# Performance work log

Hardware: AMD Instinct MI355X
Metric: run time of the kernel (lower is better)

The kernel has to match this reference:

```python
import jax, jax.numpy as jnp
import numpy as np

B, L, S, H, E = 2, 2048, 2048, 8, 64
EPS = 1e-8


def setup_inputs() -> dict:
    key = jax.random.key(0)
    k1, k2, k3, k4, k5 = jax.random.split(key, 5)
    query = jax.random.normal(k1, (B, L, H, E), jnp.float32)
    key_t = jax.random.normal(k2, (B, S, H, E), jnp.float32)
    value = jax.random.normal(k3, (B, S, H, E), jnp.float32)
    mask_miss_k = jax.random.bernoulli(k4, 0.1, (B, S, 1))
    mask_miss_q = jax.random.bernoulli(k5, 0.1, (B, L, 1))
    # ensure key position 0 is never missing so no softmax row is fully masked
    mask_miss_k = mask_miss_k.at[:, 0, :].set(False)
    pos = jnp.broadcast_to(jnp.arange(L, dtype=jnp.int32)[None, :, None], (B, L, 1))
    return {"query": query, "key": key_t, "value": value,
            "mask_miss_k": mask_miss_k, "mask_miss_q": mask_miss_q,
            "pos": pos, "causal_mask": 1}


def reference(query, key, value, mask_miss_k, mask_miss_q, pos, causal_mask):
    # query: (B,L,H,E)  key/value: (B,S,H,E)  masks: (B,S,1)/(B,L,1) bool  pos: (B,L,1)
    E_ = query.shape[-1]
    scale = 1.0 / np.sqrt(E_)
    neg_inf = jnp.float32(-jnp.inf)

    scores = jnp.einsum('blhe,bshe->bhls', query, key)  # (B,H,L,S)

    if causal_mask:
        p = pos[..., 0]  # (B,L)
        # M[b,i,j] = -inf where p_j > p_i, broadcast over heads
        m_causal = jnp.where(p[:, None, :] > p[:, :, None], neg_inf, 0.0)[:, None, :, :]
        scores = scores + m_causal

    m_k = jnp.where(mask_miss_k[..., 0][:, None, None, :], neg_inf, 0.0)  # (B,1,1,S)
    m_q = jnp.where(mask_miss_q[..., 0][:, None, :, None], neg_inf, 0.0)  # (B,1,L,1)

    att = jax.nn.relu(jax.nn.softmax(scale * (scores + m_k), axis=-1) + m_q)

    # per-row attention entropy (register_entropy=True path)
    entropy = -jnp.sum(att * jnp.log(jnp.clip(att, EPS, None)), axis=-1)  # (B,H,L)
    entropy = jnp.nan_to_num(entropy, nan=0.0)

    # dropout p=0.0 -> identity; nan_to_num as in original
    A = jnp.nan_to_num(att)
    V = jnp.einsum('bhls,bshd->blhd', A, value)  # (B,L,H,E)
    return V, A, entropy
```

## Files before the change

### kernel.cpp

```cpp
#include <hip/hip_runtime.h>

#define B_ 2
#define L_ 2048
#define S_ 2048
#define H_ 8
#define E_ 64
#define VSTRIDE 136

typedef float f32x4 __attribute__((ext_vector_type(4)));
typedef short s16x8 __attribute__((ext_vector_type(8)));
typedef unsigned int u32;
typedef unsigned short u16;
typedef unsigned long long u64;

__device__ __forceinline__ u32 bc(float f){ return __builtin_bit_cast(u32, f); }
__device__ __forceinline__ float exp2g(float x){ return __builtin_amdgcn_exp2f(x); }

__device__ __forceinline__ s16x8 pack8(f32x4 a, f32x4 b){
  union { s16x8 v; u32 w[4]; } r;
  r.w[0] = __builtin_amdgcn_perm(bc(a[1]), bc(a[0]), 0x07060302u);
  r.w[1] = __builtin_amdgcn_perm(bc(a[3]), bc(a[2]), 0x07060302u);
  r.w[2] = __builtin_amdgcn_perm(bc(b[1]), bc(b[0]), 0x07060302u);
  r.w[3] = __builtin_amdgcn_perm(bc(b[3]), bc(b[2]), 0x07060302u);
  return r.v;
}

__device__ __forceinline__ void loadK2(const float* kr, s16x8& f0, s16x8& f1){
  f32x4 a0 = *(const f32x4*)(kr);
  f32x4 a1 = *(const f32x4*)(kr + 4);
  f32x4 b0 = *(const f32x4*)(kr + 32);
  f32x4 b1 = *(const f32x4*)(kr + 36);
  f0 = pack8(a0, a1);
  f1 = pack8(b0, b1);
}

__launch_bounds__(256, 4)
__global__ void attn_kernel(const float* __restrict__ Q,
                            const float* __restrict__ K,
                            const float* __restrict__ V,
                            const int* __restrict__ maskK,
                            const int* __restrict__ maskQ,
                            const int* __restrict__ causal_p,
                            float* __restrict__ outV,
                            float* __restrict__ outA,
                            float* __restrict__ outEnt)
{
  __shared__ __align__(16) u16 vstage[64 * VSTRIDE];
  __shared__ float lsum[4][32];
  __shared__ float tsum[4][32];
  __shared__ float recipS[32];
  __shared__ __align__(8) unsigned char mkb[2048];

  const int tid  = threadIdx.x;
  const int lane = tid & 63;
  const int wv   = tid >> 6;
  const int quad = lane >> 4;
  const int l15  = lane & 15;
  const int permrow = ((l15 >> 2) << 3) | (l15 & 3);

  const int n   = blockIdx.x;
  const int s   = n >> 3;
  const int bh  = ((n & 7) << 1) | (s >> 6);
  const int b   = bh >> 3;
  const int h   = bh & 7;
  const int iA  = (s & 63) << 4;
  const int iB  = 2032 - iA;

  const int causal = causal_p[0] != 0;
  const int imaxA  = causal ? (iA + 15) : (S_ - 1);
  const int imaxB  = causal ? (iB + 15) : (S_ - 1);
  const int nsup   = (imaxB >> 7) + 1;

  {
    const int* mk = maskK + b * S_ + tid * 8;
    u32 w0 = (u32)(mk[0]!=0) | ((u32)(mk[1]!=0)<<8) | ((u32)(mk[2]!=0)<<16) | ((u32)(mk[3]!=0)<<24);
    u32 w1 = (u32)(mk[4]!=0) | ((u32)(mk[5]!=0)<<8) | ((u32)(mk[6]!=0)<<16) | ((u32)(mk[7]!=0)<<24);
    ((uint2*)mkb)[tid] = make_uint2(w0, w1);
  }

  float* const outArowA = outA + ((size_t)bh * L_ + iA) * S_;
  float* const outArowB = outA + ((size_t)bh * L_ + iB) * S_;

  if (causal){
    const f32x4 z4 = {0.f, 0.f, 0.f, 0.f};
    const int jzA = ((imaxA >> 5) + 1) << 5;
    for (int r = 0; r < 16; ++r)
      for (int c = jzA + (tid << 2); c < S_; c += 1024)
        *(f32x4*)(outArowA + (size_t)r * S_ + c) = z4;
    const int jzB = ((imaxB >> 5) + 1) << 5;
    for (int r = 0; r < 16; ++r)
      for (int c = jzB + (tid << 2); c < S_; c += 1024)
        *(f32x4*)(outArowB + (size_t)r * S_ + c) = z4;
  }

  s16x8 qfA0, qfA1, qfB0, qfB1;
  {
    const float qs = 0.125f * 1.44269504f;
    const float* qa = Q + (((size_t)(b * L_ + iA + l15)) * H_ + h) * E_;
    const float* qb = Q + (((size_t)(b * L_ + iB + l15)) * H_ + h) * E_;
    qfA0 = pack8(*(const f32x4*)(qa + quad*8) * qs,      *(const f32x4*)(qa + quad*8 + 4) * qs);
    qfA1 = pack8(*(const f32x4*)(qa + 32 + quad*8) * qs, *(const f32x4*)(qa + 32 + quad*8 + 4) * qs);
    qfB0 = pack8(*(const f32x4*)(qb + quad*8) * qs,      *(const f32x4*)(qb + quad*8 + 4) * qs);
    qfB1 = pack8(*(const f32x4*)(qb + 32 + quad*8) * qs, *(const f32x4*)(qb + 32 + quad*8 + 4) * qs);
  }

  const float* const Kbh = K + ((size_t)(b * S_) * H_ + h) * E_;
  const f32x4 zero4 = {0.f, 0.f, 0.f, 0.f};
  const int irowA = iA + l15;
  const int irowB = iB + l15;

  __syncthreads();

  float lA = 0.f, tA = 0.f, lB = 0.f, tB = 0.f;
  for (int c = wv; (c << 5) <= imaxB; c += 4){
    const int j0c = c << 5;
    s16x8 ka0, ka1, kb0, kb1;
    const float* krow = Kbh + (size_t)(j0c + permrow) * (H_ * E_) + quad * 8;
    loadK2(krow, ka0, ka1);
    loadK2(krow + 4 * (H_ * E_), kb0, kb1);
    const int jbase = j0c + (quad << 3);
    const u64 mk8 = *(const u64*)(mkb + jbase);
    const u32 mlo = (u32)mk8;
    const u32 mhi = (u32)(mk8 >> 32);
    {
      f32x4 sa = __builtin_amdgcn_mfma_f32_16x16x32_bf16(ka0, qfB0, zero4, 0, 0, 0);
      sa       = __builtin_amdgcn_mfma_f32_16x16x32_bf16(ka1, qfB1, sa, 0, 0, 0);
      f32x4 sb = __builtin_amdgcn_mfma_f32_16x16x32_bf16(kb0, qfB0, zero4, 0, 0, 0);
      sb       = __builtin_amdgcn_mfma_f32_16x16x32_bf16(kb1, qfB1, sb, 0, 0, 0);
      const int rel = irowB - jbase;
      #pragma unroll
      for (int r = 0; r < 4; ++r){
        const bool da = (((mlo >> (8*r)) & 0xffu) != 0u) || (causal && (r > rel));
        const float ea = da ? 0.f : exp2g(sa[r]);
        lB += ea; tB = __builtin_fmaf(ea, sa[r], tB);
        const bool db = (((mhi >> (8*r)) & 0xffu) != 0u) || (causal && (r + 4 > rel));
        const float eb = db ? 0.f : exp2g(sb[r]);
        lB += eb; tB = __builtin_fmaf(eb, sb[r], tB);
      }
    }
    if (j0c <= imaxA){
      f32x4 sa = __builtin_amdgcn_mfma_f32_16x16x32_bf16(ka0, qfA0, zero4, 0, 0, 0);
      sa       = __builtin_amdgcn_mfma_f32_16x16x32_bf16(ka1, qfA1, sa, 0, 0, 0);
      f32x4 sb = __builtin_amdgcn_mfma_f32_16x16x32_bf16(kb0, qfA0, zero4, 0, 0, 0);
      sb       = __builtin_amdgcn_mfma_f32_16x16x32_bf16(kb1, qfA1, sb, 0, 0, 0);
      const int rel = irowA - jbase;
      #pragma unroll
      for (int r = 0; r < 4; ++r){
        const bool da = (((mlo >> (8*r)) & 0xffu) != 0u) || (causal && (r > rel));
        const float ea = da ? 0.f : exp2g(sa[r]);
        lA += ea; tA = __builtin_fmaf(ea, sa[r], tA);
        const bool db = (((mhi >> (8*r)) & 0xffu) != 0u) || (causal && (r + 4 > rel));
        const float eb = db ? 0.f : exp2g(sb[r]);
        lA += eb; tA = __builtin_fmaf(eb, sb[r], tA);
      }
    }
  }

  #pragma unroll
  for (int off = 16; off < 64; off <<= 1){
    lA += __shfl_xor(lA, off);  tA += __shfl_xor(tA, off);
    lB += __shfl_xor(lB, off);  tB += __shfl_xor(tB, off);
  }
  if (lane < 16){
    lsum[wv][l15]      = lA;  tsum[wv][l15]      = tA;
    lsum[wv][16 + l15] = lB;  tsum[wv][16 + l15] = tB;
  }
  __syncthreads();
  if (tid < 32){
    float l = lsum[0][tid] + lsum[1][tid] + lsum[2][tid] + lsum[3][tid];
    float t = (tsum[0][tid] + tsum[1][tid] + tsum[2][tid] + tsum[3][tid]) * 0.69314718f;
    const int i0t = (tid < 16) ? iA : iB;
    const int row = i0t + (tid & 15);
    int qm = maskQ[b * L_ + row];
    float rc  = (qm != 0) ? 0.f : (1.f / l);
    float ent = (qm != 0) ? 0.f : (__logf(l) - t / l);
    recipS[tid] = rc;
    outEnt[(size_t)bh * L_ + row] = ent;
  }
  __syncthreads();

  const float rqA = recipS[l15];
  const float rqB = recipS[16 + l15];

  f32x4 uaccA[4], uaccB[4];
  #pragma unroll
  for (int et = 0; et < 4; ++et){ uaccA[et] = (f32x4)0.f; uaccB[et] = (f32x4)0.f; }

  for (int sp = 0; sp < nsup; ++sp){
    const int j0c = (sp << 7) + (wv << 5);
    if (j0c > imaxB) break;

    {
      const int jp = tid >> 2;
      const int a  = tid & 3;
      const int e0 = a << 4;
      const float* v0 = V + (((size_t)(b * S_ + (sp << 7) + 2 * jp)) * H_ + h) * E_ + e0;
      const float* v1 = v0 + H_ * E_;
      f32x4 x0 = *(const f32x4*)(v0);
      f32x4 x1 = *(const f32x4*)(v0 + 4);
      f32x4 x2 = *(const f32x4*)(v0 + 8);
      f32x4 x3 = *(const f32x4*)(v0 + 12);
      f32x4 y0 = *(const f32x4*)(v1);
      f32x4 y1 = *(const f32x4*)(v1 + 4);
      f32x4 y2 = *(const f32x4*)(v1 + 8);
      f32x4 y3 = *(const f32x4*)(v1 + 12);
      const int colsw = ((((jp >> 2) + (a << 2)) & 15) << 2) | (jp & 3);
      u32* vsw = (u32*)vstage;
      #pragma unroll
      for (int k = 0; k < 4; ++k){
        vsw[(e0 + k     ) * (VSTRIDE/2) + colsw] = __builtin_amdgcn_perm(bc(y0[k]), bc(x0[k]), 0x07060302u);
        vsw[(e0 + 4 + k ) * (VSTRIDE/2) + colsw] = __builtin_amdgcn_perm(bc(y1[k]), bc(x1[k]), 0x07060302u);
        vsw[(e0 + 8 + k ) * (VSTRIDE/2) + colsw] = __builtin_amdgcn_perm(bc(y2[k]), bc(x2[k]), 0x07060302u);
        vsw[(e0 + 12 + k) * (VSTRIDE/2) + colsw] = __builtin_amdgcn_perm(bc(y3[k]), bc(x3[k]), 0x07060302u);
      }
    }

    s16x8 ka0, ka1, kb0, kb1;
    const float* krow = Kbh + (size_t)(j0c + permrow) * (H_ * E_) + quad * 8;
    loadK2(krow, ka0, ka1);
    loadK2(krow + 4 * (H_ * E_), kb0, kb1);
    const int jbase = j0c + (quad << 3);
    const u64 mk8 = *(const u64*)(mkb + jbase);
    const u32 mlo = (u32)mk8;
    const u32 mhi = (u32)(mk8 >> 32);

    {
      f32x4 sa = __builtin_amdgcn_mfma_f32_16x16x32_bf16(ka0, qfB0, zero4, 0, 0, 0);
      sa       = __builtin_amdgcn_mfma_f32_16x16x32_bf16(ka1, qfB1, sa, 0, 0, 0);
      f32x4 sb = __builtin_amdgcn_mfma_f32_16x16x32_bf16(kb0, qfB0, zero4, 0, 0, 0);
      sb       = __builtin_amdgcn_mfma_f32_16x16x32_bf16(kb1, qfB1, sb, 0, 0, 0);
      const int rel = irowB - jbase;
      f32x4 ea, eb;
      #pragma unroll
      for (int r = 0; r < 4; ++r){
        const bool da = (((mlo >> (8*r)) & 0xffu) != 0u) || (causal && (r > rel));
        ea[r] = da ? 0.f : exp2g(sa[r]);
        const bool db = (((mhi >> (8*r)) & 0xffu) != 0u) || (causal && (r + 4 > rel));
        eb[r] = db ? 0.f : exp2g(sb[r]);
      }
      *(f32x4*)(outArowB + (size_t)l15 * S_ + jbase)     = ea * rqB;
      *(f32x4*)(outArowB + (size_t)l15 * S_ + jbase + 4) = eb * rqB;
      const s16x8 pf = pack8(ea, eb);
      #pragma unroll
      for (int et = 0; et < 4; ++et){
        const int gq = ((wv << 2) + quad + (et << 2)) & 15;
        const s16x8 vf = *(const s16x8*)(vstage + (et * 16 + l15) * VSTRIDE + gq * 8);
        uaccB[et] = __builtin_amdgcn_mfma_f32_16x16x32_bf16(pf, vf, uaccB[et], 0, 0, 0);
      }
    }

    if (j0c <= imaxA){
      f32x4 sa = __builtin_amdgcn_mfma_f32_16x16x32_bf16(ka0, qfA0, zero4, 0, 0, 0);
      sa       = __builtin_amdgcn_mfma_f32_16x16x32_bf16(ka1, qfA1, sa, 0, 0, 0);
      f32x4 sb = __builtin_amdgcn_mfma_f32_16x16x32_bf16(kb0, qfA0, zero4, 0, 0, 0);
      sb       = __builtin_amdgcn_mfma_f32_16x16x32_bf16(kb1, qfA1, sb, 0, 0, 0);
      const int rel = irowA - jbase;
      f32x4 ea, eb;
      #pragma unroll
      for (int r = 0; r < 4; ++r){
        const bool da = (((mlo >> (8*r)) & 0xffu) != 0u) || (causal && (r > rel));
        ea[r] = da ? 0.f : exp2g(sa[r]);
        const bool db = (((mhi >> (8*r)) & 0xffu) != 0u) || (causal && (r + 4 > rel));
        eb[r] = db ? 0.f : exp2g(sb[r]);
      }
      *(f32x4*)(outArowA + (size_t)l15 * S_ + jbase)     = ea * rqA;
      *(f32x4*)(outArowA + (size_t)l15 * S_ + jbase + 4) = eb * rqA;
      const s16x8 pf = pack8(ea, eb);
      #pragma unroll
      for (int et = 0; et < 4; ++et){
        const int gq = ((wv << 2) + quad + (et << 2)) & 15;
        const s16x8 vf = *(const s16x8*)(vstage + (et * 16 + l15) * VSTRIDE + gq * 8);
        uaccA[et] = __builtin_amdgcn_mfma_f32_16x16x32_bf16(pf, vf, uaccA[et], 0, 0, 0);
      }
    }
  }

  float* Ubuf = (float*)vstage;
  __syncthreads();
  #pragma unroll
  for (int et = 0; et < 4; ++et)
    #pragma unroll
    for (int r = 0; r < 4; ++r)
      Ubuf[(wv * 16 + (quad << 2) + r) * 64 + et * 16 + l15] = uaccA[et][r];
  __syncthreads();
  {
    const int i  = tid >> 4;
    const int e4 = (tid & 15) << 2;
    f32x4 s0 = *(const f32x4*)(Ubuf + (0 * 16 + i) * 64 + e4);
    f32x4 s1 = *(const f32x4*)(Ubuf + (1 * 16 + i) * 64 + e4);
    f32x4 s2 = *(const f32x4*)(Ubuf + (2 * 16 + i) * 64 + e4);
    f32x4 s3 = *(const f32x4*)(Ubuf + (3 * 16 + i) * 64 + e4);
    f32x4 vout = (s0 + s1 + s2 + s3) * recipS[i];
    *(f32x4*)(outV + (((size_t)(b * L_ + iA + i)) * H_ + h) * E_ + e4) = vout;
  }
  __syncthreads();
  #pragma unroll
  for (int et = 0; et < 4; ++et)
    #pragma unroll
    for (int r = 0; r < 4; ++r)
      Ubuf[(wv * 16 + (quad << 2) + r) * 64 + et * 16 + l15] = uaccB[et][r];
  __syncthreads();
  {
    const int i  = tid >> 4;
    const int e4 = (tid & 15) << 2;
    f32x4 s0 = *(const f32x4*)(Ubuf + (0 * 16 + i) * 64 + e4);
    f32x4 s1 = *(const f32x4*)(Ubuf + (1 * 16 + i) * 64 + e4);
    f32x4 s2 = *(const f32x4*)(Ubuf + (2 * 16 + i) * 64 + e4);
    f32x4 s3 = *(const f32x4*)(Ubuf + (3 * 16 + i) * 64 + e4);
    f32x4 vout = (s0 + s1 + s2 + s3) * recipS[16 + i];
    *(f32x4*)(outV + (((size_t)(b * L_ + iB + i)) * H_ + h) * E_ + e4) = vout;
  }
}

extern "C" void kernel_launch(void* const* d_in, const int* in_sizes, int n_in,
                              void* d_out, int out_size, void* d_ws, size_t ws_size,
                              hipStream_t stream){
  const float* Q  = (const float*)d_in[0];
  const float* K  = (const float*)d_in[1];
  const float* V  = (const float*)d_in[2];
  const int* mk   = (const int*)d_in[3];
  const int* mq   = (const int*)d_in[4];
  const int* cm   = (const int*)d_in[6];

  float* outV   = (float*)d_out;
  float* outA   = outV + (size_t)B_ * L_ * H_ * E_;
  float* outEnt = outA + (size_t)B_ * H_ * L_ * S_;

  attn_kernel<<<dim3(1024), 256, 0, stream>>>(Q, K, V, mk, mq, cm, outV, outA, outEnt);
}
```

Before: 400.7 us.

## Use 512 threads per block with eight waves splitting key columns

Doubles the block size from 4 to 8 wavefronts, so each pass of the key/value loops covers 256 columns instead of 128. The V staging buffer, the mask preload, the zero-fill stride and the cross-wave reductions are widened to match. The aim is more parallelism per query tile and fewer serial super-iterations. In exchange it needs more LDS per block, more per-wave partial sums to reduce, and the launch bound of 8 may cap registers.

New measurement: 499.9 us. 1.25x slower.

```diff
diff --git a/kernel.cpp b/kernel.cpp
--- a/kernel.cpp
+++ b/kernel.cpp
@@ -5,7 +5,7 @@
 #define S_ 2048
 #define H_ 8
 #define E_ 64
-#define VSTRIDE 136
+#define VSTRIDE 264
 
 typedef float f32x4 __attribute__((ext_vector_type(4)));
 typedef short s16x8 __attribute__((ext_vector_type(8)));
@@ -34,7 +34,7 @@
   f1 = pack8(b0, b1);
 }
 
-__launch_bounds__(256, 4)
+__launch_bounds__(512, 8)
 __global__ void attn_kernel(const float* __restrict__ Q,
                             const float* __restrict__ K,
                             const float* __restrict__ V,
@@ -46,8 +46,8 @@
                             float* __restrict__ outEnt)
 {
   __shared__ __align__(16) u16 vstage[64 * VSTRIDE];
-  __shared__ float lsum[4][32];
-  __shared__ float tsum[4][32];
+  __shared__ float lsum[8][32];
+  __shared__ float tsum[8][32];
   __shared__ float recipS[32];
   __shared__ __align__(8) unsigned char mkb[2048];
 
@@ -69,13 +69,12 @@
   const int causal = causal_p[0] != 0;
   const int imaxA  = causal ? (iA + 15) : (S_ - 1);
   const int imaxB  = causal ? (iB + 15) : (S_ - 1);
-  const int nsup   = (imaxB >> 7) + 1;
+  const int nsup   = (imaxB >> 8) + 1;
 
   {
-    const int* mk = maskK + b * S_ + tid * 8;
+    const int* mk = maskK + b * S_ + tid * 4;
     u32 w0 = (u32)(mk[0]!=0) | ((u32)(mk[1]!=0)<<8) | ((u32)(mk[2]!=0)<<16) | ((u32)(mk[3]!=0)<<24);
-    u32 w1 = (u32)(mk[4]!=0) | ((u32)(mk[5]!=0)<<8) | ((u32)(mk[6]!=0)<<16) | ((u32)(mk[7]!=0)<<24);
-    ((uint2*)mkb)[tid] = make_uint2(w0, w1);
+    ((u32*)mkb)[tid] = w0;
   }
 
   float* const outArowA = outA + ((size_t)bh * L_ + iA) * S_;
@@ -85,11 +84,11 @@
     const f32x4 z4 = {0.f, 0.f, 0.f, 0.f};
     const int jzA = ((imaxA >> 5) + 1) << 5;
     for (int r = 0; r < 16; ++r)
-      for (int c = jzA + (tid << 2); c < S_; c += 1024)
+      for (int c = jzA + (tid << 2); c < S_; c += 2048)
         *(f32x4*)(outArowA + (size_t)r * S_ + c) = z4;
     const int jzB = ((imaxB >> 5) + 1) << 5;
     for (int r = 0; r < 16; ++r)
-      for (int c = jzB + (tid << 2); c < S_; c += 1024)
+      for (int c = jzB + (tid << 2); c < S_; c += 2048)
         *(f32x4*)(outArowB + (size_t)r * S_ + c) = z4;
   }
 
@@ -112,7 +111,7 @@
   __syncthreads();
 
   float lA = 0.f, tA = 0.f, lB = 0.f, tB = 0.f;
-  for (int c = wv; (c << 5) <= imaxB; c += 4){
+  for (int c = wv; (c << 5) <= imaxB; c += 8){
     const int j0c = c << 5;
     s16x8 ka0, ka1, kb0, kb1;
     const float* krow = Kbh + (size_t)(j0c + permrow) * (H_ * E_) + quad * 8;
@@ -167,8 +166,10 @@
   }
   __syncthreads();
   if (tid < 32){
-    float l = lsum[0][tid] + lsum[1][tid] + lsum[2][tid] + lsum[3][tid];
-    float t = (tsum[0][tid] + tsum[1][tid] + tsum[2][tid] + tsum[3][tid]) * 0.69314718f;
+    float l = 0.f, t = 0.f;
+    #pragma unroll
+    for (int p = 0; p < 8; ++p){ l += lsum[p][tid]; t += tsum[p][tid]; }
+    t *= 0.69314718f;
     const int i0t = (tid < 16) ? iA : iB;
     const int row = i0t + (tid & 15);
     int qm = maskQ[b * L_ + row];
@@ -187,14 +188,14 @@
   for (int et = 0; et < 4; ++et){ uaccA[et] = (f32x4)0.f; uaccB[et] = (f32x4)0.f; }
 
   for (int sp = 0; sp < nsup; ++sp){
-    const int j0c = (sp << 7) + (wv << 5);
+    const int j0c = (sp << 8) + (wv << 5);
     if (j0c > imaxB) break;
 
     {
       const int jp = tid >> 2;
       const int a  = tid & 3;
       const int e0 = a << 4;
-      const float* v0 = V + (((size_t)(b * S_ + (sp << 7) + 2 * jp)) * H_ + h) * E_ + e0;
+      const float* v0 = V + (((size_t)(b * S_ + (sp << 8) + 2 * jp)) * H_ + h) * E_ + e0;
       const float* v1 = v0 + H_ * E_;
       f32x4 x0 = *(const f32x4*)(v0);
       f32x4 x1 = *(const f32x4*)(v0 + 4);
@@ -204,7 +205,7 @@
       f32x4 y1 = *(const f32x4*)(v1 + 4);
       f32x4 y2 = *(const f32x4*)(v1 + 8);
       f32x4 y3 = *(const f32x4*)(v1 + 12);
-      const int colsw = ((((jp >> 2) + (a << 2)) & 15) << 2) | (jp & 3);
+      const int colsw = ((((jp >> 2) + (a << 2)) & 31) << 2) | (jp & 3);
       u32* vsw = (u32*)vstage;
       #pragma unroll
       for (int k = 0; k < 4; ++k){
@@ -243,7 +244,7 @@
       const s16x8 pf = pack8(ea, eb);
       #pragma unroll
       for (int et = 0; et < 4; ++et){
-        const int gq = ((wv << 2) + quad + (et << 2)) & 15;
+        const int gq = ((wv << 2) + quad + (et << 2)) & 31;
         const s16x8 vf = *(const s16x8*)(vstage + (et * 16 + l15) * VSTRIDE + gq * 8);
         uaccB[et] = __builtin_amdgcn_mfma_f32_16x16x32_bf16(pf, vf, uaccB[et], 0, 0, 0);
       }
@@ -268,7 +269,7 @@
       const s16x8 pf = pack8(ea, eb);
       #pragma unroll
       for (int et = 0; et < 4; ++et){
-        const int gq = ((wv << 2) + quad + (et << 2)) & 15;
+        const int gq = ((wv << 2) + quad + (et << 2)) & 31;
         const s16x8 vf = *(const s16x8*)(vstage + (et * 16 + l15) * VSTRIDE + gq * 8);
         uaccA[et] = __builtin_amdgcn_mfma_f32_16x16x32_bf16(pf, vf, uaccA[et], 0, 0, 0);
       }
@@ -283,14 +284,14 @@
     for (int r = 0; r < 4; ++r)
       Ubuf[(wv * 16 + (quad << 2) + r) * 64 + et * 16 + l15] = uaccA[et][r];
   __syncthreads();
-  {
+  if (tid < 256){
     const int i  = tid >> 4;
     const int e4 = (tid & 15) << 2;
-    f32x4 s0 = *(const f32x4*)(Ubuf + (0 * 16 + i) * 64 + e4);
-    f32x4 s1 = *(const f32x4*)(Ubuf + (1 * 16 + i) * 64 + e4);
-    f32x4 s2 = *(const f32x4*)(Ubuf + (2 * 16 + i) * 64 + e4);
-    f32x4 s3 = *(const f32x4*)(Ubuf + (3 * 16 + i) * 64 + e4);
-    f32x4 vout = (s0 + s1 + s2 + s3) * recipS[i];
+    f32x4 acc = (f32x4)0.f;
+    #pragma unroll
+    for (int p = 0; p < 8; ++p)
+      acc += *(const f32x4*)(Ubuf + (p * 16 + i) * 64 + e4);
+    f32x4 vout = acc * recipS[i];
     *(f32x4*)(outV + (((size_t)(b * L_ + iA + i)) * H_ + h) * E_ + e4) = vout;
   }
   __syncthreads();
@@ -300,14 +301,14 @@
     for (int r = 0; r < 4; ++r)
       Ubuf[(wv * 16 + (quad << 2) + r) * 64 + et * 16 + l15] = uaccB[et][r];
   __syncthreads();
-  {
+  if (tid < 256){
     const int i  = tid >> 4;
     const int e4 = (tid & 15) << 2;
-    f32x4 s0 = *(const f32x4*)(Ubuf + (0 * 16 + i) * 64 + e4);
-    f32x4 s1 = *(const f32x4*)(Ubuf + (1 * 16 + i) * 64 + e4);
-    f32x4 s2 = *(const f32x4*)(Ubuf + (2 * 16 + i) * 64 + e4);
-    f32x4 s3 = *(const f32x4*)(Ubuf + (3 * 16 + i) * 64 + e4);
-    f32x4 vout = (s0 + s1 + s2 + s3) * recipS[16 + i];
+    f32x4 acc = (f32x4)0.f;
+    #pragma unroll
+    for (int p = 0; p < 8; ++p)
+      acc += *(const f32x4*)(Ubuf + (p * 16 + i) * 64 + e4);
+    f32x4 vout = acc * recipS[16 + i];
     *(f32x4*)(outV + (((size_t)(b * L_ + iB + i)) * H_ + h) * E_ + e4) = vout;
   }
 }
@@ -326,5 +327,5 @@
   float* outA   = outV + (size_t)B_ * L_ * H_ * E_;
   float* outEnt = outA + (size_t)B_ * H_ * L_ * S_;
 
-  attn_kernel<<<dim3(1024), 256, 0, stream>>>(Q, K, V, mk, mq, cm, outV, outA, outEnt);
+  attn_kernel<<<dim3(1024), 512, 0, stream>>>(Q, K, V, mk, mq, cm, outV, outA, outEnt);
 }
```

## Give each block one query tile instead of paired causal tiles, doubling grid

Applied to the files above, without the earlier changes.

Each block previously handled two 16-row query tiles (iA and its mirror iB) so causal work was balanced per block. Now each block handles a single 16-row tile, the grid doubles to 2048 blocks, and tiles are issued longest-first. The launch bound is raised to 8 blocks per SM and the V staging stride shrinks to 132. This aims for more parallelism and occupancy from fewer registers per thread. In exchange, K and V loads are no longer shared between two query tiles and per-block work is uneven, which now depends on the scheduler to balance.

After: 486.7 us. 21.4% more time.

```diff
diff --git a/kernel.cpp b/kernel.cpp
--- a/kernel.cpp
+++ b/kernel.cpp
@@ -5,7 +5,7 @@
 #define S_ 2048
 #define H_ 8
 #define E_ 64
-#define VSTRIDE 136
+#define VSTRIDE 132
 
 typedef float f32x4 __attribute__((ext_vector_type(4)));
 typedef short s16x8 __attribute__((ext_vector_type(8)));
@@ -34,7 +34,7 @@
   f1 = pack8(b0, b1);
 }
 
-__launch_bounds__(256, 4)
+__launch_bounds__(256, 8)
 __global__ void attn_kernel(const float* __restrict__ Q,
                             const float* __restrict__ K,
                             const float* __restrict__ V,
@@ -46,9 +46,9 @@
                             float* __restrict__ outEnt)
 {
   __shared__ __align__(16) u16 vstage[64 * VSTRIDE];
-  __shared__ float lsum[4][32];
-  __shared__ float tsum[4][32];
-  __shared__ float recipS[32];
+  __shared__ float lsum[4][16];
+  __shared__ float tsum[4][16];
+  __shared__ float recipS[16];
   __shared__ __align__(8) unsigned char mkb[2048];
 
   const int tid  = threadIdx.x;
@@ -60,16 +60,14 @@
 
   const int n   = blockIdx.x;
   const int s   = n >> 3;
-  const int bh  = ((n & 7) << 1) | (s >> 6);
+  const int bh  = ((n & 7) << 1) | (s >> 7);
   const int b   = bh >> 3;
   const int h   = bh & 7;
-  const int iA  = (s & 63) << 4;
-  const int iB  = 2032 - iA;
+  const int i0  = (127 - (s & 127)) << 4;
 
   const int causal = causal_p[0] != 0;
-  const int imaxA  = causal ? (iA + 15) : (S_ - 1);
-  const int imaxB  = causal ? (iB + 15) : (S_ - 1);
-  const int nsup   = (imaxB >> 7) + 1;
+  const int imax   = causal ? (i0 + 15) : (S_ - 1);
+  const int nsup   = (imax >> 7) + 1;
 
   {
     const int* mk = maskK + b * S_ + tid * 8;
@@ -78,99 +76,70 @@
     ((uint2*)mkb)[tid] = make_uint2(w0, w1);
   }
 
-  float* const outArowA = outA + ((size_t)bh * L_ + iA) * S_;
-  float* const outArowB = outA + ((size_t)bh * L_ + iB) * S_;
+  float* const outArow = outA + ((size_t)bh * L_ + i0) * S_;
 
   if (causal){
     const f32x4 z4 = {0.f, 0.f, 0.f, 0.f};
-    const int jzA = ((imaxA >> 5) + 1) << 5;
+    const int jz = ((imax >> 5) + 1) << 5;
     for (int r = 0; r < 16; ++r)
-      for (int c = jzA + (tid << 2); c < S_; c += 1024)
-        *(f32x4*)(outArowA + (size_t)r * S_ + c) = z4;
-    const int jzB = ((imaxB >> 5) + 1) << 5;
-    for (int r = 0; r < 16; ++r)
-      for (int c = jzB + (tid << 2); c < S_; c += 1024)
-        *(f32x4*)(outArowB + (size_t)r * S_ + c) = z4;
-  }
-
-  s16x8 qfA0, qfA1, qfB0, qfB1;
+      for (int c = jz + (tid << 2); c < S_; c += 1024)
+        *(f32x4*)(outArow + (size_t)r * S_ + c) = z4;
+  }
+
+  s16x8 qf0, qf1;
   {
     const float qs = 0.125f * 1.44269504f;
-    const float* qa = Q + (((size_t)(b * L_ + iA + l15)) * H_ + h) * E_;
-    const float* qb = Q + (((size_t)(b * L_ + iB + l15)) * H_ + h) * E_;
-    qfA0 = pack8(*(const f32x4*)(qa + quad*8) * qs,      *(const f32x4*)(qa + quad*8 + 4) * qs);
-    qfA1 = pack8(*(const f32x4*)(qa + 32 + quad*8) * qs, *(const f32x4*)(qa + 32 + quad*8 + 4) * qs);
-    qfB0 = pack8(*(const f32x4*)(qb + quad*8) * qs,      *(const f32x4*)(qb + quad*8 + 4) * qs);
-    qfB1 = pack8(*(const f32x4*)(qb + 32 + quad*8) * qs, *(const f32x4*)(qb + 32 + quad*8 + 4) * qs);
-  }
-
+    const float* qa = Q + (((size_t)(b * L_ + i0 + l15)) * H_ + h) * E_;
+    qf0 = pack8(*(const f32x4*)(qa + quad*8) * qs,      *(const f32x4*)(qa + quad*8 + 4) * qs);
+    qf1 = pack8(*(const f32x4*)(qa + 32 + quad*8) * qs, *(const f32x4*)(qa + 32 + quad*8 + 4) * qs);
+  }
+
+  const size_t rstride = (size_t)(H_ * E_);
   const float* const Kbh = K + ((size_t)(b * S_) * H_ + h) * E_;
   const f32x4 zero4 = {0.f, 0.f, 0.f, 0.f};
-  const int irowA = iA + l15;
-  const int irowB = iB + l15;
-
-  __syncthreads();
-
-  float lA = 0.f, tA = 0.f, lB = 0.f, tB = 0.f;
-  for (int c = wv; (c << 5) <= imaxB; c += 4){
+  const int irow = i0 + l15;
+
+  __syncthreads();
+
+  float lacc = 0.f, tacc = 0.f;
+  for (int c = wv; (c << 5) <= imax; c += 4){
     const int j0c = c << 5;
     s16x8 ka0, ka1, kb0, kb1;
-    const float* krow = Kbh + (size_t)(j0c + permrow) * (H_ * E_) + quad * 8;
+    const float* krow = Kbh + (size_t)(j0c + permrow) * rstride + quad * 8;
     loadK2(krow, ka0, ka1);
-    loadK2(krow + 4 * (H_ * E_), kb0, kb1);
+    loadK2(krow + 4 * rstride, kb0, kb1);
     const int jbase = j0c + (quad << 3);
     const u64 mk8 = *(const u64*)(mkb + jbase);
     const u32 mlo = (u32)mk8;
     const u32 mhi = (u32)(mk8 >> 32);
-    {
-      f32x4 sa = __builtin_amdgcn_mfma_f32_16x16x32_bf16(ka0, qfB0, zero4, 0, 0, 0);
-      sa       = __builtin_amdgcn_mfma_f32_16x16x32_bf16(ka1, qfB1, sa, 0, 0, 0);
-      f32x4 sb = __builtin_amdgcn_mfma_f32_16x16x32_bf16(kb0, qfB0, zero4, 0, 0, 0);
-      sb       = __builtin_amdgcn_mfma_f32_16x16x32_bf16(kb1, qfB1, sb, 0, 0, 0);
-      const int rel = irowB - jbase;
-      #pragma unroll
-      for (int r = 0; r < 4; ++r){
-        const bool da = (((mlo >> (8*r)) & 0xffu) != 0u) || (causal && (r > rel));
-        const float ea = da ? 0.f : exp2g(sa[r]);
-        lB += ea; tB = __builtin_fmaf(ea, sa[r], tB);
-        const bool db = (((mhi >> (8*r)) & 0xffu) != 0u) || (causal && (r + 4 > rel));
-        const float eb = db ? 0.f : exp2g(sb[r]);
-        lB += eb; tB = __builtin_fmaf(eb, sb[r], tB);
-      }
-    }
-    if (j0c <= imaxA){
-      f32x4 sa = __builtin_amdgcn_mfma_f32_16x16x32_bf16(ka0, qfA0, zero4, 0, 0, 0);
-      sa       = __builtin_amdgcn_mfma_f32_16x16x32_bf16(ka1, qfA1, sa, 0, 0, 0);
-      f32x4 sb = __builtin_amdgcn_mfma_f32_16x16x32_bf16(kb0, qfA0, zero4, 0, 0, 0);
-      sb       = __builtin_amdgcn_mfma_f32_16x16x32_bf16(kb1, qfA1, sb, 0, 0, 0);
-      const int rel = irowA - jbase;
-      #pragma unroll
-      for (int r = 0; r < 4; ++r){
-        const bool da = (((mlo >> (8*r)) & 0xffu) != 0u) || (causal && (r > rel));
-        const float ea = da ? 0.f : exp2g(sa[r]);
-        lA += ea; tA = __builtin_fmaf(ea, sa[r], tA);
-        const bool db = (((mhi >> (8*r)) & 0xffu) != 0u) || (causal && (r + 4 > rel));
-        const float eb = db ? 0.f : exp2g(sb[r]);
-        lA += eb; tA = __builtin_fmaf(eb, sb[r], tA);
-      }
+    f32x4 sa = __builtin_amdgcn_mfma_f32_16x16x32_bf16(ka0, qf0, zero4, 0, 0, 0);
+    sa       = __builtin_amdgcn_mfma_f32_16x16x32_bf16(ka1, qf1, sa, 0, 0, 0);
+    f32x4 sb = __builtin_amdgcn_mfma_f32_16x16x32_bf16(kb0, qf0, zero4, 0, 0, 0);
+    sb       = __builtin_amdgcn_mfma_f32_16x16x32_bf16(kb1, qf1, sb, 0, 0, 0);
+    const int rel = irow - jbase;
+    #pragma unroll
+    for (int r = 0; r < 4; ++r){
+      const bool da = (((mlo >> (8*r)) & 0xffu) != 0u) || (causal && (r > rel));
+      const float ea = da ? 0.f : exp2g(sa[r]);
+      lacc += ea; tacc = __builtin_fmaf(ea, sa[r], tacc);
+      const bool db = (((mhi >> (8*r)) & 0xffu) != 0u) || (causal && (r + 4 > rel));
+      const float eb = db ? 0.f : exp2g(sb[r]);
+      lacc += eb; tacc = __builtin_fmaf(eb, sb[r], tacc);
     }
   }
 
   #pragma unroll
   for (int off = 16; off < 64; off <<= 1){
-    lA += __shfl_xor(lA, off);  tA += __shfl_xor(tA, off);
-    lB += __shfl_xor(lB, off);  tB += __shfl_xor(tB, off);
+    lacc += __shfl_xor(lacc, off);  tacc += __shfl_xor(tacc, off);
   }
   if (lane < 16){
-    lsum[wv][l15]      = lA;  tsum[wv][l15]      = tA;
-    lsum[wv][16 + l15] = lB;  tsum[wv][16 + l15] = tB;
-  }
-  __syncthreads();
-  if (tid < 32){
+    lsum[wv][l15] = lacc;  tsum[wv][l15] = tacc;
+  }
+  __syncthreads();
+  if (tid < 16){
     float l = lsum[0][tid] + lsum[1][tid] + lsum[2][tid] + lsum[3][tid];
     float t = (tsum[0][tid] + tsum[1][tid] + tsum[2][tid] + tsum[3][tid]) * 0.69314718f;
-    const int i0t = (tid < 16) ? iA : iB;
-    const int row = i0t + (tid & 15);
+    const int row = i0 + tid;
     int qm = maskQ[b * L_ + row];
     float rc  = (qm != 0) ? 0.f : (1.f / l);
     float ent = (qm != 0) ? 0.f : (__logf(l) - t / l);
@@ -179,16 +148,15 @@
   }
   __syncthreads();
 
-  const float rqA = recipS[l15];
-  const float rqB = recipS[16 + l15];
-
-  f32x4 uaccA[4], uaccB[4];
+  const float rq = recipS[l15];
+
+  f32x4 uacc[4];
   #pragma unroll
-  for (int et = 0; et < 4; ++et){ uaccA[et] = (f32x4)0.f; uaccB[et] = (f32x4)0.f; }
+  for (int et = 0; et < 4; ++et) uacc[et] = (f32x4)0.f;
 
   for (int sp = 0; sp < nsup; ++sp){
     const int j0c = (sp << 7) + (wv << 5);
-    if (j0c > imaxB) break;
+    if (j0c > imax) break;
 
     {
       const int jp = tid >> 2;
@@ -216,62 +184,36 @@
     }
 
     s16x8 ka0, ka1, kb0, kb1;
-    const float* krow = Kbh + (size_t)(j0c + permrow) * (H_ * E_) + quad * 8;
+    const float* krow = Kbh + (size_t)(j0c + permrow) * rstride + quad * 8;
     loadK2(krow, ka0, ka1);
-    loadK2(krow + 4 * (H_ * E_), kb0, kb1);
+    loadK2(krow + 4 * rstride, kb0, kb1);
     const int jbase = j0c + (quad << 3);
     const u64 mk8 = *(const u64*)(mkb + jbase);
     const u32 mlo = (u32)mk8;
     const u32 mhi = (u32)(mk8 >> 32);
 
-    {
-      f32x4 sa = __builtin_amdgcn_mfma_f32_16x16x32_bf16(ka0, qfB0, zero4, 0, 0, 0);
-      sa       = __builtin_amdgcn_mfma_f32_16x16x32_bf16(ka1, qfB1, sa, 0, 0, 0);
-      f32x4 sb = __builtin_amdgcn_mfma_f32_16x16x32_bf16(kb0, qfB0, zero4, 0, 0, 0);
-      sb       = __builtin_amdgcn_mfma_f32_16x16x32_bf16(kb1, qfB1, sb, 0, 0, 0);
-      const int rel = irowB - jbase;
-      f32x4 ea, eb;
-      #pragma unroll
-      for (int r = 0; r < 4; ++r){
-        const bool da = (((mlo >> (8*r)) & 0xffu) != 0u) || (causal && (r > rel));
-        ea[r] = da ? 0.f : exp2g(sa[r]);
-        const bool db = (((mhi >> (8*r)) & 0xffu) != 0u) || (causal && (r + 4 > rel));
-        eb[r] = db ? 0.f : exp2g(sb[r]);
-      }
-      *(f32x4*)(outArowB + (size_t)l15 * S_ + jbase)     = ea * rqB;
-      *(f32x4*)(outArowB + (size_t)l15 * S_ + jbase + 4) = eb * rqB;
-      const s16x8 pf = pack8(ea, eb);
-      #pragma unroll
-      for (int et = 0; et < 4; ++et){
-        const int gq = ((wv << 2) + quad + (et << 2)) & 15;
-        const s16x8 vf = *(const s16x8*)(vstage + (et * 16 + l15) * VSTRIDE + gq * 8);
-        uaccB[et] = __builtin_amdgcn_mfma_f32_16x16x32_bf16(pf, vf, uaccB[et], 0, 0, 0);
-      }
-    }
-
-    if (j0c <= imaxA){
-      f32x4 sa = __builtin_amdgcn_mfma_f32_16x16x32_bf16(ka0, qfA0, zero4, 0, 0, 0);
-      sa       = __builtin_amdgcn_mfma_f32_16x16x32_bf16(ka1, qfA1, sa, 0, 0, 0);
-      f32x4 sb = __builtin_amdgcn_mfma_f32_16x16x32_bf16(kb0, qfA0, zero4, 0, 0, 0);
-      sb       = __builtin_amdgcn_mfma_f32_16x16x32_bf16(kb1, qfA1, sb, 0, 0, 0);
-      const int rel = irowA - jbase;
-      f32x4 ea, eb;
-      #pragma unroll
-      for (int r = 0; r < 4; ++r){
-        const bool da = (((mlo >> (8*r)) & 0xffu) != 0u) || (causal && (r > rel));
-        ea[r] = da ? 0.f : exp2g(sa[r]);
-        const bool db = (((mhi >> (8*r)) & 0xffu) != 0u) || (causal && (r + 4 > rel));
-        eb[r] = db ? 0.f : exp2g(sb[r]);
-      }
-      *(f32x4*)(outArowA + (size_t)l15 * S_ + jbase)     = ea * rqA;
-      *(f32x4*)(outArowA + (size_t)l15 * S_ + jbase + 4) = eb * rqA;
-      const s16x8 pf = pack8(ea, eb);
-      #pragma unroll
-      for (int et = 0; et < 4; ++et){
-        const int gq = ((wv << 2) + quad + (et << 2)) & 15;
-        const s16x8 vf = *(const s16x8*)(vstage + (et * 16 + l15) * VSTRIDE + gq * 8);
-        uaccA[et] = __builtin_amdgcn_mfma_f32_16x16x32_bf16(pf, vf, uaccA[et], 0, 0, 0);
-      }
+    f32x4 sa = __builtin_amdgcn_mfma_f32_16x16x32_bf16(ka0, qf0, zero4, 0, 0, 0);
+    sa       = __builtin_amdgcn_mfma_f32_16x16x32_bf16(ka1, qf1, sa, 0, 0, 0);
+    f32x4 sb = __builtin_amdgcn_mfma_f32_16x16x32_bf16(kb0, qf0, zero4, 0, 0, 0);
+    sb       = __builtin_amdgcn_mfma_f32_16x16x32_bf16(kb1, qf1, sb, 0, 0, 0);
+    const int rel = irow - jbase;
+    f32x4 ea, eb;
+    #pragma unroll
+    for (int r = 0; r < 4; ++r){
+      const bool da = (((mlo >> (8*r)) & 0xffu) != 0u) || (causal && (r > rel));
+      ea[r] = da ? 0.f : exp2g(sa[r]);
+      const bool db = (((mhi >> (8*r)) & 0xffu) != 0u) || (causal && (r + 4 > rel));
+      eb[r] = db ? 0.f : exp2g(sb[r]);
+    }
+    *(f32x4*)(outArow + (size_t)l15 * S_ + jbase)     = ea * rq;
+    *(f32x4*)(outArow + (size_t)l15 * S_ + jbase + 4) = eb * rq;
+    const s16x8 pf = pack8(ea, eb);
+
+    #pragma unroll
+    for (int et = 0; et < 4; ++et){
+      const int gq = ((wv << 2) + quad + (et << 2)) & 15;
+      const s16x8 vf = *(const s16x8*)(vstage + (et * 16 + l15) * VSTRIDE + gq * 8);
+      uacc[et] = __builtin_amdgcn_mfma_f32_16x16x32_bf16(pf, vf, uacc[et], 0, 0, 0);
     }
   }
 
@@ -281,7 +223,7 @@
   for (int et = 0; et < 4; ++et)
     #pragma unroll
     for (int r = 0; r < 4; ++r)
-      Ubuf[(wv * 16 + (quad << 2) + r) * 64 + et * 16 + l15] = uaccA[et][r];
+      Ubuf[(wv * 16 + (quad << 2) + r) * 64 + et * 16 + l15] = uacc[et][r];
   __syncthreads();
   {
     const int i  = tid >> 4;
@@ -291,24 +233,7 @@
     f32x4 s2 = *(const f32x4*)(Ubuf + (2 * 16 + i) * 64 + e4);
     f32x4 s3 = *(const f32x4*)(Ubuf + (3 * 16 + i) * 64 + e4);
     f32x4 vout = (s0 + s1 + s2 + s3) * recipS[i];
-    *(f32x4*)(outV + (((size_t)(b * L_ + iA + i)) * H_ + h) * E_ + e4) = vout;
-  }
-  __syncthreads();
-  #pragma unroll
-  for (int et = 0; et < 4; ++et)
-    #pragma unroll
-    for (int r = 0; r < 4; ++r)
-      Ubuf[(wv * 16 + (quad << 2) + r) * 64 + et * 16 + l15] = uaccB[et][r];
-  __syncthreads();
-  {
-    const int i  = tid >> 4;
-    const int e4 = (tid & 15) << 2;
-    f32x4 s0 = *(const f32x4*)(Ubuf + (0 * 16 + i) * 64 + e4);
-    f32x4 s1 = *(const f32x4*)(Ubuf + (1 * 16 + i) * 64 + e4);
-    f32x4 s2 = *(const f32x4*)(Ubuf + (2 * 16 + i) * 64 + e4);
-    f32x4 s3 = *(const f32x4*)(Ubuf + (3 * 16 + i) * 64 + e4);
-    f32x4 vout = (s0 + s1 + s2 + s3) * recipS[16 + i];
-    *(f32x4*)(outV + (((size_t)(b * L_ + iB + i)) * H_ + h) * E_ + e4) = vout;
+    *(f32x4*)(outV + (((size_t)(b * L_ + i0 + i)) * H_ + h) * E_ + e4) = vout;
   }
 }
 
@@ -326,5 +251,5 @@
   float* outA   = outV + (size_t)B_ * L_ * H_ * E_;
   float* outEnt = outA + (size_t)B_ * H_ * L_ * S_;
 
-  attn_kernel<<<dim3(1024), 256, 0, stream>>>(Q, K, V, mk, mq, cm, outV, outA, outEnt);
-}
+  attn_kernel<<<dim3(2048), 256, 0, stream>>>(Q, K, V, mk, mq, cm, outV, outA, outEnt);
+}
```
